# Performance work log

Hardware: AMD Instinct MI355X
Metric: run time of the kernel (lower is better)

## Reference

```python
import jax, jax.numpy as jnp
import numpy as np


def setup_inputs() -> dict:
    key = jax.random.key(0)
    ks = jax.random.split(key, 6)
    b, l, d, n, r = 2, 2048, 512, 64, 32
    x = jax.random.normal(ks[0], (b, l, d), dtype=jnp.float32)
    # x_proj: Linear(d, r + 2n, bias=False) -> weight (r+2n, d)
    W_xproj = jax.random.normal(ks[1], (r + 2 * n, d), dtype=jnp.float32) / np.sqrt(d)
    # dt_proj: Linear(r, d, bias=True)
    W_dt = jax.random.normal(ks[2], (d, r), dtype=jnp.float32) / np.sqrt(r)
    b_dt = jax.random.normal(ks[3], (d,), dtype=jnp.float32) * 0.01
    # A_log = log(repeat(arange(1, n+1), 'n -> d n'))
    A_log = jnp.log(jnp.broadcast_to(jnp.arange(1, n + 1, dtype=jnp.float32), (d, n)))
    D = jnp.ones((d,), dtype=jnp.float32)
    return {"x": x, "W_xproj": W_xproj, "W_dt": W_dt, "b_dt": b_dt, "A_log": A_log, "D": D}


def _s6_forward(x, W_xproj, W_dt, b_dt, A_log, D):
    d, n = A_log.shape
    r = W_dt.shape[1]
    A = -jnp.exp(A_log)                               # (d, n)
    x_dbl = jnp.einsum('bld,ed->ble', x, W_xproj)     # (b, l, r+2n)
    delta_r = x_dbl[..., :r]
    B = x_dbl[..., r:r + n]                           # (b, l, n)
    C = x_dbl[..., r + n:]                            # (b, l, n)
    delta = jax.nn.softplus(jnp.einsum('blr,dr->bld', delta_r, W_dt) + b_dt)  # (b, l, d)
    # discretize
    deltaA = jnp.exp(jnp.einsum('bld,dn->bldn', delta, A))        # (b, l, d, n)
    deltaB_u = jnp.einsum('bld,bln,bld->bldn', delta, B, x)       # (b, l, d, n)
    bsz = x.shape[0]
    h0 = jnp.zeros((bsz, d, n), dtype=x.dtype)

    def step(h, inp):
        dA_t, dBu_t, C_t = inp                        # (b,d,n), (b,d,n), (b,n)
        h = dA_t * h + dBu_t
        y_t = jnp.einsum('bdn,bn->bd', h, C_t)
        return h, y_t

    xs = (jnp.moveaxis(deltaA, 1, 0), jnp.moveaxis(deltaB_u, 1, 0), jnp.moveaxis(C, 1, 0))
    _, ys = jax.lax.scan(step, h0, xs)                # ys: (l, b, d)
    y = jnp.moveaxis(ys, 0, 1)                        # (b, l, d)
    return y + x * D


def reference(x, W_xproj, W_dt, b_dt, A_log, D):
    return _s6_forward(x, W_xproj, W_dt, b_dt, A_log, D)
```

## Files before the change

kernel.cpp:

```cpp
#include <hip/hip_runtime.h>
#include <cstdint>

#define Bsz 2
#define Lsz 2048
#define Dm  512
#define Nst 64
#define Rr  32
#define Ee  160
#define NCHUNK 64
#define CLEN   32
#define L2E 1.44269504f
#define LN2 0.69314718f

typedef __bf16  bf16x8 __attribute__((ext_vector_type(8)));
typedef float   f32x4  __attribute__((ext_vector_type(4)));
typedef unsigned short u16x8 __attribute__((ext_vector_type(8)));

__device__ __forceinline__ float rdlane(float v, int l) {
    return __int_as_float(__builtin_amdgcn_readlane(__float_as_int(v), l));
}
__device__ __forceinline__ float fexp2(float x) { return __builtin_amdgcn_exp2f(x); }
__device__ __forceinline__ float flog2(float x) { return __builtin_amdgcn_logf(x); }

__global__ __launch_bounds__(256) void kcast2(const float* __restrict__ a,
                                              unsigned short* __restrict__ oa, int na8,
                                              const float* __restrict__ b,
                                              unsigned short* __restrict__ ob, int nb8) {
    int gid = blockIdx.x * 256 + threadIdx.x;
    const float* in; unsigned short* op; int idx;
    if (gid < na8) { in = a; op = oa; idx = gid; }
    else { idx = gid - na8; if (idx >= nb8) return; in = b; op = ob; }
    const float4* ip = reinterpret_cast<const float4*>(in) + (size_t)idx * 2;
    float4 v0 = ip[0], v1 = ip[1];
    float vv[8] = {v0.x, v0.y, v0.z, v0.w, v1.x, v1.y, v1.z, v1.w};
    u16x8 r;
    #pragma unroll
    for (int j = 0; j < 8; ++j) {
        uint32_t u = __float_as_uint(vv[j]);
        u += 0x7FFFu + ((u >> 16) & 1u);
        r[j] = (unsigned short)(u >> 16);
    }
    *reinterpret_cast<u16x8*>(op + (size_t)idx * 8) = r;
}

__global__ __launch_bounds__(256) void k1_mfma(const unsigned short* __restrict__ xbf,
                                               const unsigned short* __restrict__ wbf,
                                               float* __restrict__ xdbl) {
    const int tid = threadIdx.x;
    const int wv = tid >> 6, lane = tid & 63;
    const int ng = blockIdx.x % 10, mg = blockIdx.x / 10;
    const int m0 = mg * 64 + wv * 16;
    const int n0 = ng * 16;
    const int ra = lane & 15, kg = lane >> 4;
    const unsigned short* ap = xbf + (size_t)(m0 + ra) * Dm + kg * 8;
    const unsigned short* bp = wbf + (size_t)(n0 + ra) * Dm + kg * 8;
    f32x4 acc = {0.f, 0.f, 0.f, 0.f};
    #pragma unroll
    for (int ks = 0; ks < 16; ++ks) {
        bf16x8 a = *reinterpret_cast<const bf16x8*>(ap + ks * 32);
        bf16x8 b = *reinterpret_cast<const bf16x8*>(bp + ks * 32);
        acc = __builtin_amdgcn_mfma_f32_16x16x32_bf16(a, b, acc, 0, 0, 0);
    }
    float* dp = xdbl + (size_t)(m0 + kg * 4) * Ee + n0 + ra;
    dp[0]      = acc[0];
    dp[Ee]     = acc[1];
    dp[2 * Ee] = acc[2];
    dp[3 * Ee] = acc[3];
}

__global__ __launch_bounds__(256) void k2_delta(const float* __restrict__ xdbl,
                                                const float* __restrict__ x,
                                                const float* __restrict__ Wdt,
                                                const float* __restrict__ bdt,
                                                float* __restrict__ delta_t,
                                                float* __restrict__ du_t,
                                                float* __restrict__ sumdl) {
    __shared__ float dr[64][33];
    __shared__ float wd[64][32];
    __shared__ float pt[64][65];
    const int tid = threadIdx.x;
    const int lt = blockIdx.x & 31;
    const int dt = (blockIdx.x >> 5) & 7;
    const int b  = blockIdx.x >> 8;
    const int l0 = lt * 64, d0 = dt * 64;

    for (int i = tid; i < 512; i += 256) {
        int l = i >> 3, j4 = i & 7;
        const float4 v = *reinterpret_cast<const float4*>(
            xdbl + (size_t)(b * Lsz + l0 + l) * Ee + j4 * 4);
        dr[l][j4 * 4 + 0] = v.x; dr[l][j4 * 4 + 1] = v.y;
        dr[l][j4 * 4 + 2] = v.z; dr[l][j4 * 4 + 3] = v.w;
    }
    for (int i = tid; i < 512; i += 256) {
        int dd = i >> 3, j4 = i & 7;
        *reinterpret_cast<float4*>(&wd[dd][j4 * 4]) =
            *reinterpret_cast<const float4*>(Wdt + (size_t)(d0 + dd) * Rr + j4 * 4);
    }
    __syncthreads();

    const int w = tid >> 6, lane = tid & 63;
    float drr[32];
    #pragma unroll
    for (int j = 0; j < 32; ++j) drr[j] = dr[lane][j];

    float xv[16];
    {
        const float* xp = x + (size_t)(b * Lsz + l0 + lane) * Dm + d0 + w * 16;
        #pragma unroll
        for (int q = 0; q < 4; ++q) {
            float4 v = reinterpret_cast<const float4*>(xp)[q];
            xv[q*4] = v.x; xv[q*4+1] = v.y; xv[q*4+2] = v.z; xv[q*4+3] = v.w;
        }
    }

    float dl[16];
    #pragma unroll
    for (int i = 0; i < 16; ++i) {
        int dd = w * 16 + i;
        float z = bdt[d0 + dd];
        const float4* wr = reinterpret_cast<const float4*>(&wd[dd][0]);
        #pragma unroll
        for (int j4 = 0; j4 < 8; ++j4) {
            float4 wv = wr[j4];
            z = fmaf(drr[j4*4+0], wv.x, z);
            z = fmaf(drr[j4*4+1], wv.y, z);
            z = fmaf(drr[j4*4+2], wv.z, z);
            z = fmaf(drr[j4*4+3], wv.w, z);
        }
        float t = fexp2(-fabsf(z) * L2E);
        dl[i] = fmaxf(z, 0.f) + flog2(1.f + t) * LN2;
    }

    #pragma unroll
    for (int i = 0; i < 16; ++i) pt[w * 16 + i][lane] = dl[i];
    __syncthreads();
    for (int i = tid; i < 4096; i += 256) {
        int dd = i >> 6, ll = i & 63;
        delta_t[((size_t)(b * Dm + d0 + dd)) * Lsz + l0 + ll] = pt[dd][ll];
    }
    if (tid < 64) {
        float s0 = 0.f, s1 = 0.f;
        #pragma unroll 16
        for (int q = 0; q < 32; ++q) { s0 += pt[tid][q]; s1 += pt[tid][32 + q]; }
        size_t sb = (size_t)(b * Dm + d0 + tid) * NCHUNK + lt * 2;
        sumdl[sb] = s0; sumdl[sb + 1] = s1;
    }
    __syncthreads();
    #pragma unroll
    for (int i = 0; i < 16; ++i) pt[w * 16 + i][lane] = dl[i] * xv[i];
    __syncthreads();
    for (int i = tid; i < 4096; i += 256) {
        int dd = i >> 6, ll = i & 63;
        du_t[((size_t)(b * Dm + d0 + dd)) * Lsz + l0 + ll] = pt[dd][ll];
    }
}

__global__ __launch_bounds__(256) void k3a(const float* __restrict__ delta_t,
                                           const float* __restrict__ du_t,
                                           const float* __restrict__ xdbl,
                                           const float* __restrict__ Alog,
                                           float* __restrict__ hf) {
    __shared__ float Bs[32][64];
    const int tid = threadIdx.x;
    const int w = __builtin_amdgcn_readfirstlane(tid >> 6);
    const int lane = tid & 63;
    const int c   = blockIdx.x & 63;
    const int grp = blockIdx.x >> 6;
    const int chan0 = grp * 16 + w * 4;
    const int b = chan0 >> 9;
    const int t0 = c * CLEN;
    const float* __restrict__ xb0 = xdbl + ((size_t)b * Lsz + t0) * Ee;
    for (int i = tid; i < 512; i += 256) {
        int row = i >> 4, q = i & 15;
        float4 v = *reinterpret_cast<const float4*>(xb0 + row * Ee + Rr + q * 4);
        *reinterpret_cast<float4*>(&Bs[row][q * 4]) = v;
    }
    const int tl = lane & 31;
    float A2[4], h[4], dpack[4];
    #pragma unroll
    for (int ch = 0; ch < 4; ++ch) {
        const int cc = chan0 + ch;
        A2[ch] = -expf(Alog[(size_t)(cc & 511) * Nst + lane]) * L2E;
        dpack[ch] = (lane < 32) ? delta_t[(size_t)cc * Lsz + t0 + tl]
                                : du_t   [(size_t)cc * Lsz + t0 + tl];
        h[ch] = 0.f;
    }
    __syncthreads();
    #pragma unroll 8
    for (int j = 0; j < CLEN; ++j) {
        float Bv = Bs[j][lane];
        #pragma unroll
        for (int ch = 0; ch < 4; ++ch) {
            float sd = rdlane(dpack[ch], j);
            float su = rdlane(dpack[ch], 32 + j);
            h[ch] = fmaf(fexp2(sd * A2[ch]), h[ch], su * Bv);
        }
    }
    #pragma unroll
    for (int ch = 0; ch < 4; ++ch)
        hf[((size_t)(chan0 + ch) * NCHUNK + c) * Nst + lane] = h[ch];
}

__global__ __launch_bounds__(256) void k3b(const float* __restrict__ Alog,
                                           const float* __restrict__ sumdl,
                                           float* __restrict__ hf) {
    const int tid = threadIdx.x;
    const int w = tid >> 6, lane = tid & 63;
    const int chan = blockIdx.x * 4 + w;
    const int d = chan & 511;
    const float A2 = -expf(Alog[(size_t)d * Nst + lane]) * L2E;
    const float sv = sumdl[chan * NCHUNK + lane];
    const size_t base = (size_t)chan * NCHUNK * Nst + lane;
    float hv[8], nx[8];
    #pragma unroll
    for (int i = 0; i < 8; ++i) hv[i] = hf[base + i * Nst];
    float h0 = 0.f;
    for (int g = 0; g < 8; ++g) {
        if (g < 7) {
            #pragma unroll
            for (int i = 0; i < 8; ++i) nx[i] = hf[base + ((g + 1) * 8 + i) * Nst];
        }
        #pragma unroll
        for (int i = 0; i < 8; ++i) {
            const int c = g * 8 + i;
            float P = fexp2(A2 * rdlane(sv, c));
            hf[base + c * Nst] = h0;
            h0 = fmaf(P, h0, hv[i]);
        }
        #pragma unroll
        for (int i = 0; i < 8; ++i) hv[i] = nx[i];
    }
}

__global__ __launch_bounds__(256, 6) void k3c(const float* __restrict__ delta_t,
                                              const float* __restrict__ du_t,
                                              const float* __restrict__ xdbl,
                                              const float* __restrict__ Alog,
                                              const float* __restrict__ h0s,
                                              const float* __restrict__ x,
                                              const float* __restrict__ Dv,
                                              float* __restrict__ out) {
    __shared__ float BC[16][128];
    __shared__ float part[4][8][68];
    __shared__ float ystage[4][8][34];
    const int tid = threadIdx.x;
    const int w = __builtin_amdgcn_readfirstlane(tid >> 6);
    const int lane = tid & 63;
    const int c   = blockIdx.x & 63;
    const int grp = blockIdx.x >> 6;
    const int chan0 = grp * 32 + w * 8;
    const int b = chan0 >> 9;
    const int t0 = c * CLEN;
    const float* __restrict__ xb0 = xdbl + ((size_t)b * Lsz + t0) * Ee + Rr;

    const int tl = lane & 31;
    float A2[8], h[8], dpack[8];
    #pragma unroll
    for (int ch = 0; ch < 8; ++ch) {
        const int cc = chan0 + ch;
        A2[ch] = -expf(Alog[(size_t)(cc & 511) * Nst + lane]) * L2E;
        dpack[ch] = (lane < 32) ? delta_t[(size_t)cc * Lsz + t0 + tl]
                                : du_t   [(size_t)cc * Lsz + t0 + tl];
        h[ch] = h0s[((size_t)cc * NCHUNK + c) * Nst + lane];
    }
    const int r8 = lane & 7, sg = lane >> 3;
    const int srow = tid >> 5, scol = (tid & 31) * 4;

    float4 pf0 = *reinterpret_cast<const float4*>(xb0 + srow * Ee + scol);
    float4 pf1 = *reinterpret_cast<const float4*>(xb0 + (srow + 8) * Ee + scol);

    for (int q = 0; q < 2; ++q) {
        __syncthreads();
        *reinterpret_cast<float4*>(&BC[srow][scol]) = pf0;
        *reinterpret_cast<float4*>(&BC[srow + 8][scol]) = pf1;
        if (q < 1) {
            pf0 = *reinterpret_cast<const float4*>(xb0 + (16 + srow) * Ee + scol);
            pf1 = *reinterpret_cast<const float4*>(xb0 + (16 + srow + 8) * Ee + scol);
        }
        __syncthreads();
        #pragma unroll
        for (int tt = 0; tt < 16; ++tt) {
            const int t = q * 16 + tt;
            float4 pa, pb;
            const bool doRed = (tt > 0) || (q > 0);
            if (doRed) {
                pa = *reinterpret_cast<const float4*>(&part[w][r8][sg * 8]);
                pb = *reinterpret_cast<const float4*>(&part[w][r8][sg * 8 + 4]);
            }
            float Bv = BC[tt][lane];
            float Cv = BC[tt][64 + lane];
            #pragma unroll
            for (int ch = 0; ch < 8; ++ch) {
                float sd = rdlane(dpack[ch], t);
                float su = rdlane(dpack[ch], 32 + t);
                h[ch] = fmaf(fexp2(sd * A2[ch]), h[ch], su * Bv);
                part[w][ch][lane] = h[ch] * Cv;
            }
            if (doRed) {
                float v = ((pa.x + pa.y) + (pa.z + pa.w)) + ((pb.x + pb.y) + (pb.z + pb.w));
                v += __shfl_xor(v, 8);
                v += __shfl_xor(v, 16);
                v += __shfl_xor(v, 32);
                if (lane < 8) ystage[w][lane][t - 1] = v;
            }
        }
    }
    {
        float4 pa = *reinterpret_cast<const float4*>(&part[w][r8][sg * 8]);
        float4 pb = *reinterpret_cast<const float4*>(&part[w][r8][sg * 8 + 4]);
        float v = ((pa.x + pa.y) + (pa.z + pa.w)) + ((pb.x + pb.y) + (pb.z + pb.w));
        v += __shfl_xor(v, 8); v += __shfl_xor(v, 16); v += __shfl_xor(v, 32);
        if (lane < 8) ystage[w][lane][31] = v;
    }
    __syncthreads();
    const int d0 = (grp * 32) & 511;
    for (int i = tid; i < 1024; i += 256) {
        int t = i >> 5, dd = i & 31;
        size_t gi = ((size_t)(b * Lsz + t0 + t)) * Dm + d0 + dd;
        out[gi] = ystage[dd >> 3][dd & 7][t] + x[gi] * Dv[d0 + dd];
    }
}

extern "C" void kernel_launch(void* const* d_in, const int* in_sizes, int n_in,
                              void* d_out, int out_size, void* d_ws, size_t ws_size,
                              hipStream_t stream) {
    const float* x    = (const float*)d_in[0];
    const float* Wxp  = (const float*)d_in[1];
    const float* Wdt  = (const float*)d_in[2];
    const float* bdt  = (const float*)d_in[3];
    const float* Alog = (const float*)d_in[4];
    const float* Dv   = (const float*)d_in[5];
    float* out = (float*)d_out;

    float* ws = (float*)d_ws;
    float*          xdbl    = ws;
    float*          hf      = ws + 655360;
    unsigned short* xbf     = (unsigned short*)(ws + 655360);
    unsigned short* wbf     = (unsigned short*)(ws + 1703936);
    float*          delta_t = ws + 4849664;
    float*          du_t    = ws + 6946816;
    float*          sumdl   = ws + 9043968;

    hipLaunchKernelGGL(kcast2,  dim3(1064), dim3(256), 0, stream, x, xbf, 262144, Wxp, wbf, 10240);
    hipLaunchKernelGGL(k1_mfma, dim3(640),  dim3(256), 0, stream, xbf, wbf, xdbl);
    hipLaunchKernelGGL(k2_delta,dim3(512),  dim3(256), 0, stream, xdbl, x, Wdt, bdt, delta_t, du_t, sumdl);
    hipLaunchKernelGGL(k3a,     dim3(4096), dim3(256), 0, stream, delta_t, du_t, xdbl, Alog, hf);
    hipLaunchKernelGGL(k3b,     dim3(256),  dim3(256), 0, stream, Alog, sumdl, hf);
    hipLaunchKernelGGL(k3c,     dim3(2048), dim3(256), 0, stream, delta_t, du_t, xdbl, Alog, hf, x, Dv, out);
}
```

Baseline: 117.3 us.

## Pack delta and delta*u as bf16 pairs into one word; widen k3a channels per wave

k2 now stores delta and delta*x rounded to bf16 and packed into a single 32-bit word, replacing two fp32 intermediate arrays. This halves the write traffic in k2 and the reads in k3a/k3c, and drops one shared-memory round trip and barrier. k3a now handles 8 channels per wave with half as many blocks, which gives more independent recurrences per lane. The cost is bf16 precision on delta and du inside the scan, a risk to accuracy, and higher register pressure in k3a.

```diff
diff --git a/kernel.cpp b/kernel.cpp
--- a/kernel.cpp
+++ b/kernel.cpp
@@ -21,6 +21,11 @@
 }
 __device__ __forceinline__ float fexp2(float x) { return __builtin_amdgcn_exp2f(x); }
 __device__ __forceinline__ float flog2(float x) { return __builtin_amdgcn_logf(x); }
+__device__ __forceinline__ uint32_t bf16r(float f) {
+    uint32_t u = __float_as_uint(f);
+    u += 0x7FFFu + ((u >> 16) & 1u);
+    return u >> 16;
+}
 
 __global__ __launch_bounds__(256) void kcast2(const float* __restrict__ a,
                                               unsigned short* __restrict__ oa, int na8,
@@ -35,11 +40,7 @@
     float vv[8] = {v0.x, v0.y, v0.z, v0.w, v1.x, v1.y, v1.z, v1.w};
     u16x8 r;
     #pragma unroll
-    for (int j = 0; j < 8; ++j) {
-        uint32_t u = __float_as_uint(vv[j]);
-        u += 0x7FFFu + ((u >> 16) & 1u);
-        r[j] = (unsigned short)(u >> 16);
-    }
+    for (int j = 0; j < 8; ++j) r[j] = (unsigned short)bf16r(vv[j]);
     *reinterpret_cast<u16x8*>(op + (size_t)idx * 8) = r;
 }
 
@@ -72,8 +73,7 @@
                                                 const float* __restrict__ x,
                                                 const float* __restrict__ Wdt,
                                                 const float* __restrict__ bdt,
-                                                float* __restrict__ delta_t,
-                                                float* __restrict__ du_t,
+                                                float* __restrict__ ddt,
                                                 float* __restrict__ sumdl) {
     __shared__ float dr[64][33];
     __shared__ float wd[64][32];
@@ -132,31 +132,29 @@
     }
 
     #pragma unroll
-    for (int i = 0; i < 16; ++i) pt[w * 16 + i][lane] = dl[i];
+    for (int i = 0; i < 16; ++i) {
+        uint32_t db = bf16r(dl[i]);
+        uint32_t ub = bf16r(dl[i] * xv[i]);
+        pt[w * 16 + i][lane] = __uint_as_float(db | (ub << 16));
+    }
     __syncthreads();
     for (int i = tid; i < 4096; i += 256) {
         int dd = i >> 6, ll = i & 63;
-        delta_t[((size_t)(b * Dm + d0 + dd)) * Lsz + l0 + ll] = pt[dd][ll];
+        ddt[((size_t)(b * Dm + d0 + dd)) * Lsz + l0 + ll] = pt[dd][ll];
     }
     if (tid < 64) {
         float s0 = 0.f, s1 = 0.f;
         #pragma unroll 16
-        for (int q = 0; q < 32; ++q) { s0 += pt[tid][q]; s1 += pt[tid][32 + q]; }
+        for (int q = 0; q < 32; ++q) {
+            s0 += __uint_as_float(__float_as_uint(pt[tid][q]) << 16);
+            s1 += __uint_as_float(__float_as_uint(pt[tid][32 + q]) << 16);
+        }
         size_t sb = (size_t)(b * Dm + d0 + tid) * NCHUNK + lt * 2;
         sumdl[sb] = s0; sumdl[sb + 1] = s1;
     }
-    __syncthreads();
-    #pragma unroll
-    for (int i = 0; i < 16; ++i) pt[w * 16 + i][lane] = dl[i] * xv[i];
-    __syncthreads();
-    for (int i = tid; i < 4096; i += 256) {
-        int dd = i >> 6, ll = i & 63;
-        du_t[((size_t)(b * Dm + d0 + dd)) * Lsz + l0 + ll] = pt[dd][ll];
-    }
-}
-
-__global__ __launch_bounds__(256) void k3a(const float* __restrict__ delta_t,
-                                           const float* __restrict__ du_t,
+}
+
+__global__ __launch_bounds__(256) void k3a(const float* __restrict__ ddt,
                                            const float* __restrict__ xdbl,
                                            const float* __restrict__ Alog,
                                            float* __restrict__ hf) {
@@ -166,7 +164,7 @@
     const int lane = tid & 63;
     const int c   = blockIdx.x & 63;
     const int grp = blockIdx.x >> 6;
-    const int chan0 = grp * 16 + w * 4;
+    const int chan0 = grp * 32 + w * 8;
     const int b = chan0 >> 9;
     const int t0 = c * CLEN;
     const float* __restrict__ xb0 = xdbl + ((size_t)b * Lsz + t0) * Ee;
@@ -176,13 +174,12 @@
         *reinterpret_cast<float4*>(&Bs[row][q * 4]) = v;
     }
     const int tl = lane & 31;
-    float A2[4], h[4], dpack[4];
-    #pragma unroll
-    for (int ch = 0; ch < 4; ++ch) {
+    float A2[8], h[8], dpack[8];
+    #pragma unroll
+    for (int ch = 0; ch < 8; ++ch) {
         const int cc = chan0 + ch;
         A2[ch] = -expf(Alog[(size_t)(cc & 511) * Nst + lane]) * L2E;
-        dpack[ch] = (lane < 32) ? delta_t[(size_t)cc * Lsz + t0 + tl]
-                                : du_t   [(size_t)cc * Lsz + t0 + tl];
+        dpack[ch] = ddt[(size_t)cc * Lsz + t0 + tl];
         h[ch] = 0.f;
     }
     __syncthreads();
@@ -190,14 +187,15 @@
     for (int j = 0; j < CLEN; ++j) {
         float Bv = Bs[j][lane];
         #pragma unroll
-        for (int ch = 0; ch < 4; ++ch) {
-            float sd = rdlane(dpack[ch], j);
-            float su = rdlane(dpack[ch], 32 + j);
+        for (int ch = 0; ch < 8; ++ch) {
+            uint32_t wb = __float_as_uint(rdlane(dpack[ch], j));
+            float sd = __uint_as_float(wb << 16);
+            float su = __uint_as_float(wb & 0xffff0000u);
             h[ch] = fmaf(fexp2(sd * A2[ch]), h[ch], su * Bv);
         }
     }
     #pragma unroll
-    for (int ch = 0; ch < 4; ++ch)
+    for (int ch = 0; ch < 8; ++ch)
         hf[((size_t)(chan0 + ch) * NCHUNK + c) * Nst + lane] = h[ch];
 }
 
@@ -232,8 +230,7 @@
     }
 }
 
-__global__ __launch_bounds__(256, 6) void k3c(const float* __restrict__ delta_t,
-                                              const float* __restrict__ du_t,
+__global__ __launch_bounds__(256, 6) void k3c(const float* __restrict__ ddt,
                                               const float* __restrict__ xdbl,
                                               const float* __restrict__ Alog,
                                               const float* __restrict__ h0s,
@@ -259,8 +256,7 @@
     for (int ch = 0; ch < 8; ++ch) {
         const int cc = chan0 + ch;
         A2[ch] = -expf(Alog[(size_t)(cc & 511) * Nst + lane]) * L2E;
-        dpack[ch] = (lane < 32) ? delta_t[(size_t)cc * Lsz + t0 + tl]
-                                : du_t   [(size_t)cc * Lsz + t0 + tl];
+        dpack[ch] = ddt[(size_t)cc * Lsz + t0 + tl];
         h[ch] = h0s[((size_t)cc * NCHUNK + c) * Nst + lane];
     }
     const int r8 = lane & 7, sg = lane >> 3;
@@ -291,8 +287,9 @@
             float Cv = BC[tt][64 + lane];
             #pragma unroll
             for (int ch = 0; ch < 8; ++ch) {
-                float sd = rdlane(dpack[ch], t);
-                float su = rdlane(dpack[ch], 32 + t);
+                uint32_t wb = __float_as_uint(rdlane(dpack[ch], t));
+                float sd = __uint_as_float(wb << 16);
+                float su = __uint_as_float(wb & 0xffff0000u);
                 h[ch] = fmaf(fexp2(sd * A2[ch]), h[ch], su * Bv);
                 part[w][ch][lane] = h[ch] * Cv;
             }
@@ -337,14 +334,13 @@
     float*          hf      = ws + 655360;
     unsigned short* xbf     = (unsigned short*)(ws + 655360);
     unsigned short* wbf     = (unsigned short*)(ws + 1703936);
-    float*          delta_t = ws + 4849664;
-    float*          du_t    = ws + 6946816;
-    float*          sumdl   = ws + 9043968;
+    float*          ddt     = ws + 4849664;
+    float*          sumdl   = ws + 6946816;
 
     hipLaunchKernelGGL(kcast2,  dim3(1064), dim3(256), 0, stream, x, xbf, 262144, Wxp, wbf, 10240);
     hipLaunchKernelGGL(k1_mfma, dim3(640),  dim3(256), 0, stream, xbf, wbf, xdbl);
-    hipLaunchKernelGGL(k2_delta,dim3(512),  dim3(256), 0, stream, xdbl, x, Wdt, bdt, delta_t, du_t, sumdl);
-    hipLaunchKernelGGL(k3a,     dim3(4096), dim3(256), 0, stream, delta_t, du_t, xdbl, Alog, hf);
+    hipLaunchKernelGGL(k2_delta,dim3(512),  dim3(256), 0, stream, xdbl, x, Wdt, bdt, ddt, sumdl);
+    hipLaunchKernelGGL(k3a,     dim3(2048), dim3(256), 0, stream, ddt, xdbl, Alog, hf);
     hipLaunchKernelGGL(k3b,     dim3(256),  dim3(256), 0, stream, Alog, sumdl, hf);
-    hipLaunchKernelGGL(k3c,     dim3(2048), dim3(256), 0, stream, delta_t, du_t, xdbl, Alog, hf, x, Dv, out);
-}
+    hipLaunchKernelGGL(k3c,     dim3(2048), dim3(256), 0, stream, ddt, xdbl, Alog, hf, x, Dv, out);
+}
```

Measured after the change: 106.2 us, median of 2. 1.1x faster.
